# Kernel tuning notes

Hardware: AMD Instinct MI355X
Metric: run time of the kernel (lower is better)

## Reference

```python
import jax, jax.numpy as jnp
import numpy as np

N = 50000
E = 800000
NODE_F = 128
LIN = 128
HID = 32
HEADS = 2
OUT = 64
NCLS = 8
NEG_SLOPE = 0.2


def _lin_params(key, fan_in, fan_out, scale=0.05):
    k1, k2 = jax.random.split(key)
    W = jax.random.normal(k1, (fan_in, fan_out), jnp.float32) * scale
    b = jax.random.normal(k2, (fan_out,), jnp.float32) * scale
    return W, b


def setup_inputs() -> dict:
    key = jax.random.key(0)
    ks = jax.random.split(key, 12)
    h = jax.random.normal(ks[0], (N, NODE_F), jnp.float32)
    edge_w = jax.random.uniform(ks[1], (E,), jnp.float32, 1e-3, 1.0)
    src = jax.random.randint(ks[2], (E,), 0, N, jnp.int32)
    dst = jax.random.randint(ks[3], (E,), 0, N, jnp.int32)
    Wn, bn = _lin_params(ks[4], NODE_F, LIN)
    W1s, b1s = _lin_params(ks[5], LIN, HEADS * HID)
    W1d, b1d = _lin_params(ks[6], LIN, HEADS * HID)
    attn1 = jax.random.normal(ks[7], (HEADS, HID), jnp.float32) * 0.05
    W2s, b2s = _lin_params(ks[8], HEADS * HID, OUT)
    W2d, b2d = _lin_params(ks[9], HEADS * HID, OUT)
    attn2 = jax.random.normal(ks[10], (1, OUT), jnp.float32) * 0.05
    k11, k12, k13 = jax.random.split(ks[11], 3)
    Wc1, bc1 = _lin_params(k11, OUT, OUT // 2)
    Wc2, bc2 = _lin_params(k12, OUT // 2, OUT // 4)
    Wcls, bcls = _lin_params(k13, 2 * (OUT // 4), NCLS)
    return dict(h=h, edge_w=edge_w, src=src, dst=dst, Wn=Wn, bn=bn,
                W1s=W1s, b1s=b1s, W1d=W1d, b1d=b1d, attn1=attn1,
                W2s=W2s, b2s=b2s, W2d=W2d, b2d=b2d, attn2=attn2,
                Wc1=Wc1, bc1=bc1, Wc2=Wc2, bc2=bc2, Wcls=Wcls, bcls=bcls)


def _segment_softmax(logits, seg, num_segments):
    # logits: [E, H], seg: [E] destination node ids
    m = jax.ops.segment_max(logits, seg, num_segments=num_segments)
    e = jnp.exp(logits - m[seg])
    s = jax.ops.segment_sum(e, seg, num_segments=num_segments)
    return e / s[seg]


def _gatv2(x, src, dst, Ws, bs, Wd, bd, attn, heads, dim):
    n = x.shape[0]
    fs = (x @ Ws + bs).reshape(n, heads, dim)
    fd = (x @ Wd + bd).reshape(n, heads, dim)
    e = jax.nn.leaky_relu(fs[src] + fd[dst], NEG_SLOPE)  # [E,H,D]
    logits = jnp.einsum('ehd,hd->eh', e, attn)
    alpha = _segment_softmax(logits, dst, n)  # [E,H]
    return jax.ops.segment_sum(fs[src] * alpha[..., None], dst, num_segments=n)


def _forward(h, edge_w, src, dst, Wn, bn, W1s, b1s, W1d, b1d, attn1,
             W2s, b2s, W2d, b2d, attn2, Wc1, bc1, Wc2, bc2, Wcls, bcls):
    n = h.shape[0]
    # EdgeWeightNorm(norm='both'): w / sqrt(out_wdeg(src) * in_wdeg(dst))
    out_wdeg = jax.ops.segment_sum(edge_w, src, num_segments=n)
    in_wdeg = jax.ops.segment_sum(edge_w, dst, num_segments=n)
    norm_w = edge_w * jax.lax.rsqrt(out_wdeg[src]) * jax.lax.rsqrt(in_wdeg[dst])

    node_f = h @ Wn + bn
    # GATv2 layer 1 (dropout is identity in eval)
    g1 = _gatv2(node_f, src, dst, W1s, b1s, W1d, b1d, attn1, HEADS, HID)
    x = jax.nn.elu(g1).reshape(n, HEADS * HID)
    # GATv2 layer 2 (single head)
    g2 = _gatv2(x, src, dst, W2s, b2s, W2d, b2d, attn2, 1, OUT)
    x = jax.nn.elu(g2).reshape(n, OUT)

    # GraphConv norm='none' with edge_weight: sum_in(w * (xW)[src]) + b
    xm = x @ Wc1
    c1 = jax.ops.segment_sum(xm[src] * norm_w[:, None], dst, num_segments=n) + bc1
    x = jax.nn.elu(c1)

    # GraphConv norm='both' (unweighted degrees, clamped to >=1)
    ones_e = jnp.ones((src.shape[0],), x.dtype)
    dout = jnp.clip(jax.ops.segment_sum(ones_e, src, num_segments=n), 1.0)
    din = jnp.clip(jax.ops.segment_sum(ones_e, dst, num_segments=n), 1.0)
    xs = (x @ Wc2) * jax.lax.rsqrt(dout)[:, None]
    c2 = jax.ops.segment_sum(xs[src], dst, num_segments=n) * jax.lax.rsqrt(din)[:, None] + bc2
    x = jax.nn.elu(c2)

    # MLPPredictor: per-edge score from concat(src, dst) features
    score = jnp.concatenate([x[src], x[dst]], axis=1) @ Wcls + bcls
    return score


def reference(h, edge_w, src, dst, Wn, bn, W1s, b1s, W1d, b1d, attn1,
              W2s, b2s, W2d, b2d, attn2, Wc1, bc1, Wc2, bc2, Wcls, bcls):
    return _forward(h, edge_w, src, dst, Wn, bn, W1s, b1s, W1d, b1d, attn1,
                    W2s, b2s, W2d, b2d, attn2, Wc1, bc1, Wc2, bc2, Wcls, bcls)
```

## Files before the change

kernel.cpp:

```cpp
#include <hip/hip_runtime.h>
#include <math.h>

#define NN 50000
#define NE 800000

__device__ __forceinline__ float elu1(float x) { return x > 0.f ? x : expm1f(x); }
__device__ __forceinline__ float lrelu(float x) { return x >= 0.f ? x : 0.2f * x; }

__global__ __launch_bounds__(256) void fat0_kernel(
    const float* __restrict__ Wn, const float* __restrict__ bn,
    const float* __restrict__ W1s, const float* __restrict__ b1s,
    const float* __restrict__ W1d, const float* __restrict__ b1d,
    float* __restrict__ Wns, float* __restrict__ Wnd,
    float* __restrict__ bns, float* __restrict__ bnd,
    float* __restrict__ zbase) {
  if (blockIdx.x < 65) {
    int t = blockIdx.x * 256 + threadIdx.x;
    if (t < 8192) {
      int i = t >> 6, o = t & 63;
      float acc = 0.f;
      for (int k = 0; k < 128; ++k) acc += Wn[i * 128 + k] * W1s[k * 64 + o];
      Wns[t] = acc;
    } else if (t < 16384) {
      int u = t - 8192;
      int i = u >> 6, o = u & 63;
      float acc = 0.f;
      for (int k = 0; k < 128; ++k) acc += Wn[i * 128 + k] * W1d[k * 64 + o];
      Wnd[u] = acc;
    } else if (t < 16448) {
      int o = t - 16384;
      float acc = b1s[o];
      for (int k = 0; k < 128; ++k) acc += bn[k] * W1s[k * 64 + o];
      bns[o] = acc;
    } else if (t < 16512) {
      int o = t - 16448;
      float acc = b1d[o];
      for (int k = 0; k < 128; ++k) acc += bn[k] * W1d[k * 64 + o];
      bnd[o] = acc;
    }
  } else {
    int i = (blockIdx.x - 65) * 256 + threadIdx.x;
    if (i < 3 * NN) zbase[i] = 0.f;
  }
}

__global__ __launch_bounds__(256) void edge_rank(const int* __restrict__ dst,
                                                 int* __restrict__ cnt,
                                                 int* __restrict__ rank) {
  int e = blockIdx.x * blockDim.x + threadIdx.x;
  if (e >= NE) return;
  rank[e] = atomicAdd(&cnt[dst[e]], 1);
}

__global__ __launch_bounds__(1024) void scan_all(const int* __restrict__ cnt,
                                                 int* __restrict__ row_start) {
  __shared__ int sh[1024];
  int t = threadIdx.x;
  const int CHUNK = (NN + 1023) / 1024;
  int base = t * CHUNK;
  int lim = base + CHUNK;
  if (lim > NN) lim = NN;
  int s = 0;
#pragma unroll 8
  for (int i = base; i < lim; ++i) s += cnt[i];
  sh[t] = s;
  __syncthreads();
  for (int off = 1; off < 1024; off <<= 1) {
    int add = (t >= off) ? sh[t - off] : 0;
    __syncthreads();
    sh[t] += add;
    __syncthreads();
  }
  int run = sh[t] - s;
#pragma unroll 8
  for (int i = base; i < lim; ++i) {
    row_start[i] = run;
    run += cnt[i];
  }
  if (base < NN && base + CHUNK >= NN) row_start[NN] = run;
}

template <int K, int M, bool ELU_IN, int RS, bool DUAL>
__device__ __forceinline__ void gemm_body(int blk, float* __restrict__ xs,
                                          const float* __restrict__ X,
                                          const float* __restrict__ W1,
                                          const float* __restrict__ b1,
                                          const float* __restrict__ W2,
                                          const float* __restrict__ b2,
                                          const float* __restrict__ cnt,
                                          float* __restrict__ Y1,
                                          float* __restrict__ Y2) {
  constexpr int RPT = 4;
  constexpr int ROWS = (256 / M) * RPT;
  int row0 = blk * ROWS;
  int t = threadIdx.x;
  for (int idx = t; idx < ROWS * K; idx += 256) {
    int r = idx / K, k = idx - r * K;
    int row = row0 + r;
    float v = (row < NN) ? X[row * K + k] : 0.f;
    if (ELU_IN) v = elu1(v);
    xs[r * K + k] = v;
  }
  __syncthreads();
  int m = t % M, rg = t / M;
  int rbase = rg * RPT;
  float acc1[RPT], acc2[RPT];
#pragma unroll
  for (int j = 0; j < RPT; ++j) {
    acc1[j] = b1 ? b1[m] : 0.f;
    if (DUAL) acc2[j] = b2 ? b2[m] : 0.f;
  }
#pragma unroll 4
  for (int k = 0; k < K; ++k) {
    float w1 = W1[k * M + m];
    float w2 = DUAL ? W2[k * M + m] : 0.f;
#pragma unroll
    for (int j = 0; j < RPT; ++j) {
      float x = xs[(rbase + j) * K + k];
      acc1[j] += x * w1;
      if (DUAL) acc2[j] += x * w2;
    }
  }
#pragma unroll
  for (int j = 0; j < RPT; ++j) {
    int row = row0 + rbase + j;
    if (row >= NN) continue;
    float sc = 1.f;
    if (RS == 1) sc = rsqrtf(fmaxf(cnt[row], 1.f));
    if (RS == 2) {
      float wv = cnt[row];
      sc = (wv > 0.f) ? rsqrtf(wv) : 0.f;
    }
    Y1[row * M + m] = acc1[j] * sc;
    if (DUAL) Y2[row * M + m] = acc2[j] * sc;
  }
}

template <int K, int M, bool ELU_IN, int RS, bool DUAL>
__global__ __launch_bounds__(256) void node_gemm(const float* __restrict__ X,
                                                 const float* __restrict__ W1,
                                                 const float* __restrict__ b1,
                                                 const float* __restrict__ W2,
                                                 const float* __restrict__ b2,
                                                 const float* __restrict__ cnt,
                                                 float* __restrict__ Y1,
                                                 float* __restrict__ Y2) {
  __shared__ float xs[(256 / M) * 4 * K];
  gemm_body<K, M, ELU_IN, RS, DUAL>(blockIdx.x, xs, X, W1, b1, W2, b2, cnt, Y1, Y2);
}

__global__ __launch_bounds__(256) void fatB_kernel(
    const int* __restrict__ src, const int* __restrict__ dst,
    const float* __restrict__ ew, const int* __restrict__ row_start,
    const int* __restrict__ rank, int2* __restrict__ psrcw,
    unsigned long long* __restrict__ degw,
    const float* __restrict__ h, const float* __restrict__ Wns,
    const float* __restrict__ bns, const float* __restrict__ Wnd,
    const float* __restrict__ bnd, float* __restrict__ FS, float* __restrict__ FD) {
  __shared__ float xs[16 * 128];
  int c = blockIdx.x >> 1;
  if (blockIdx.x & 1) {
    gemm_body<128, 64, false, 0, true>(c, xs, h, Wns, bns, Wnd, bnd, nullptr, FS, FD);
  } else {
    int e = c * 256 + threadIdx.x;
    if (e >= NE) return;
    int s = src[e], d = dst[e];
    float w = ew[e];
    psrcw[row_start[d] + rank[e]] = make_int2(s, __float_as_int(w));
    unsigned long long pk = (1ULL << 44) | (unsigned long long)(w * 4294967296.0f);
    atomicAdd(&degw[s], pk);
  }
}

__global__ __launch_bounds__(256) void fatL2_kernel(
    const float* __restrict__ G, const float* __restrict__ W2s,
    const float* __restrict__ b2s, const float* __restrict__ W2d,
    const float* __restrict__ b2d, float* __restrict__ FS, float* __restrict__ FD,
    const unsigned long long* __restrict__ degw, float* __restrict__ deg) {
  __shared__ float xs[16 * 64];
  if (blockIdx.x < 3125) {
    gemm_body<64, 64, true, 0, true>(blockIdx.x, xs, G, W2s, b2s, W2d, b2d, nullptr, FS, FD);
  } else {
    int i = (blockIdx.x - 3125) * 256 + threadIdx.x;
    if (i >= NN) return;
    unsigned long long v = degw[i];
    deg[i] = (float)((double)(v & ((1ULL << 44) - 1)) * (1.0 / 4294967296.0));
    deg[NN + i] = (float)(v >> 44);
  }
}

template <int HALFW>
__global__ __launch_bounds__(256) void gat_fused(const int* __restrict__ row_start,
                                                 const int2* __restrict__ psrcw,
                                                 const float* __restrict__ fs,
                                                 const float* __restrict__ fd,
                                                 const float* __restrict__ attn,
                                                 float* __restrict__ g) {
  int n = blockIdx.x * 4 + (threadIdx.x >> 6);
  if (n >= NN) return;
  int lane = threadIdx.x & 63;
  int beg = row_start[n], end = row_start[n + 1];
  float fdv = fd[n * 64 + lane];
  float av = attn[lane];
  float acc = 0.f, den = 0.f;
  int i = beg;
  for (; i + 3 < end; i += 4) {
    int s0 = psrcw[i].x, s1 = psrcw[i + 1].x, s2 = psrcw[i + 2].x, s3 = psrcw[i + 3].x;
    float f0 = fs[s0 * 64 + lane];
    float f1 = fs[s1 * 64 + lane];
    float f2 = fs[s2 * 64 + lane];
    float f3 = fs[s3 * 64 + lane];
    float v0 = lrelu(f0 + fdv) * av;
    float v1 = lrelu(f1 + fdv) * av;
    float v2 = lrelu(f2 + fdv) * av;
    float v3 = lrelu(f3 + fdv) * av;
#pragma unroll
    for (int m = 16; m >= 1; m >>= 1) {
      v0 += __shfl_xor(v0, m, 64);
      v1 += __shfl_xor(v1, m, 64);
      v2 += __shfl_xor(v2, m, 64);
      v3 += __shfl_xor(v3, m, 64);
    }
    if (!HALFW) {
      v0 += __shfl_xor(v0, 32, 64);
      v1 += __shfl_xor(v1, 32, 64);
      v2 += __shfl_xor(v2, 32, 64);
      v3 += __shfl_xor(v3, 32, 64);
    }
    float p0 = __expf(v0);
    float p1 = __expf(v1);
    float p2 = __expf(v2);
    float p3 = __expf(v3);
    acc += f0 * p0 + f1 * p1 + f2 * p2 + f3 * p3;
    den += p0 + p1 + p2 + p3;
  }
  for (; i < end; ++i) {
    int s = psrcw[i].x;
    float fsv = fs[s * 64 + lane];
    float v = lrelu(fsv + fdv) * av;
#pragma unroll
    for (int m = 16; m >= 1; m >>= 1) v += __shfl_xor(v, m, 64);
    if (!HALFW) v += __shfl_xor(v, 32, 64);
    float p = __expf(v);
    acc += fsv * p;
    den += p;
  }
  g[n * 64 + lane] = (end > beg) ? acc / den : 0.f;
}

__global__ __launch_bounds__(256) void gconv1_fused(const int* __restrict__ row_start,
                                                    const int2* __restrict__ psrcw,
                                                    const float* __restrict__ ym,
                                                    const float* __restrict__ bc1,
                                                    float* __restrict__ x3a) {
  int n = blockIdx.x * 4 + (threadIdx.x >> 6);
  if (n >= NN) return;
  int lane = threadIdx.x & 63;
  int half = lane >> 5, f = lane & 31;
  int beg = row_start[n], end = row_start[n + 1];
  float acc = 0.f, wsum = 0.f;
  int i = beg + half;
  for (; i + 2 < end; i += 4) {
    int2 a = psrcw[i], b = psrcw[i + 2];
    float wa = __int_as_float(a.y), wb = __int_as_float(b.y);
    acc += ym[a.x * 32 + f] * wa + ym[b.x * 32 + f] * wb;
    wsum += wa + wb;
  }
  if (i < end) {
    int2 a = psrcw[i];
    float wa = __int_as_float(a.y);
    acc += ym[a.x * 32 + f] * wa;
    wsum += wa;
  }
  acc += __shfl_xor(acc, 32, 64);
  wsum += __shfl_xor(wsum, 32, 64);
  if (lane < 32) {
    float r = (end > beg) ? acc * rsqrtf(wsum) : 0.f;
    x3a[n * 32 + lane] = elu1(r + bc1[lane]);
  }
}

__global__ __launch_bounds__(256) void gconv2_fused(const int* __restrict__ row_start,
                                                    const int2* __restrict__ psrcw,
                                                    const float* __restrict__ xs,
                                                    const float* __restrict__ bc2,
                                                    float* __restrict__ x4) {
  int n = blockIdx.x * 4 + (threadIdx.x >> 6);
  if (n >= NN) return;
  int lane = threadIdx.x & 63;
  int q = lane >> 4, f = lane & 15;
  int beg = row_start[n], end = row_start[n + 1];
  float acc = 0.f;
  int i = beg + q;
  for (; i + 4 < end; i += 8) acc += xs[psrcw[i].x * 16 + f] + xs[psrcw[i + 4].x * 16 + f];
  if (i < end) acc += xs[psrcw[i].x * 16 + f];
  acc += __shfl_xor(acc, 16, 64);
  acc += __shfl_xor(acc, 32, 64);
  if (lane < 16) {
    float len = (float)(end - beg);
    x4[n * 16 + lane] = elu1(acc * rsqrtf(fmaxf(len, 1.f)) + bc2[lane]);
  }
}

__global__ __launch_bounds__(256) void classifier_kernel(const int* __restrict__ src,
                                                         const int* __restrict__ dst,
                                                         const float* __restrict__ x4,
                                                         const float* __restrict__ Wcls,
                                                         const float* __restrict__ bcls,
                                                         float* __restrict__ out) {
  __shared__ float w[256];
  __shared__ float bb[8];
  if (threadIdx.x < 256) w[threadIdx.x] = Wcls[threadIdx.x];
  if (threadIdx.x < 8) bb[threadIdx.x] = bcls[threadIdx.x];
  __syncthreads();
  int t = blockIdx.x * blockDim.x + threadIdx.x;
  int e = t >> 1, c0 = (t & 1) * 4;
  if (e >= NE) return;
  int s = src[e], d = dst[e];
  const float4* xsv = (const float4*)&x4[s * 16];
  const float4* xdv = (const float4*)&x4[d * 16];
  float acc0 = bb[c0], acc1 = bb[c0 + 1], acc2 = bb[c0 + 2], acc3 = bb[c0 + 3];
#pragma unroll
  for (int q = 0; q < 4; ++q) {
    float4 xv = xsv[q];
#pragma unroll
    for (int j = 0; j < 4; ++j) {
      float x = j == 0 ? xv.x : j == 1 ? xv.y : j == 2 ? xv.z : xv.w;
      const float* wr = &w[(q * 4 + j) * 8 + c0];
      acc0 += x * wr[0];
      acc1 += x * wr[1];
      acc2 += x * wr[2];
      acc3 += x * wr[3];
    }
  }
#pragma unroll
  for (int q = 0; q < 4; ++q) {
    float4 xv = xdv[q];
#pragma unroll
    for (int j = 0; j < 4; ++j) {
      float x = j == 0 ? xv.x : j == 1 ? xv.y : j == 2 ? xv.z : xv.w;
      const float* wr = &w[(16 + q * 4 + j) * 8 + c0];
      acc0 += x * wr[0];
      acc1 += x * wr[1];
      acc2 += x * wr[2];
      acc3 += x * wr[3];
    }
  }
  *(float4*)&out[e * 8 + c0] = make_float4(acc0, acc1, acc2, acc3);
}

extern "C" void kernel_launch(void* const* d_in, const int* in_sizes, int n_in,
                              void* d_out, int out_size, void* d_ws, size_t ws_size,
                              hipStream_t stream) {
  const float* h      = (const float*)d_in[0];
  const float* edge_w = (const float*)d_in[1];
  const int*   src    = (const int*)d_in[2];
  const int*   dst    = (const int*)d_in[3];
  const float* Wn    = (const float*)d_in[4];
  const float* bn    = (const float*)d_in[5];
  const float* W1s   = (const float*)d_in[6];
  const float* b1s   = (const float*)d_in[7];
  const float* W1d   = (const float*)d_in[8];
  const float* b1d   = (const float*)d_in[9];
  const float* attn1 = (const float*)d_in[10];
  const float* W2s   = (const float*)d_in[11];
  const float* b2s   = (const float*)d_in[12];
  const float* W2d   = (const float*)d_in[13];
  const float* b2d   = (const float*)d_in[14];
  const float* attn2 = (const float*)d_in[15];
  const float* Wc1   = (const float*)d_in[16];
  const float* bc1   = (const float*)d_in[17];
  const float* Wc2   = (const float*)d_in[18];
  const float* bc2   = (const float*)d_in[19];
  const float* Wcls  = (const float*)d_in[20];
  const float* bcls  = (const float*)d_in[21];
  float* out = (float*)d_out;

  float* ws = (float*)d_ws;
  size_t off = 0;
  auto alloc = [&](size_t nf) { float* pp = ws + off; off += (nf + 3) & ~(size_t)3; return pp; };
  float* Wns = alloc(8192);
  float* Wnd = alloc(8192);
  float* bns = alloc(64);
  float* bnd = alloc(64);
  unsigned long long* degw = (unsigned long long*)alloc(2 * NN);
  int*   cnt = (int*)alloc(NN);
  float* deg = alloc(2 * NN);
  int*   row_start = (int*)alloc(NN + 1);
  int2*  psrcw = (int2*)alloc(2 * NE);
  float* FS  = alloc(64 * NN);
  float* FD  = alloc(64 * NN);
  float* G   = alloc(64 * NN);
  int*   rank = (int*)G;

  dim3 b256(256);
  const int EB = (NE + 255) / 256;
  const int NB4 = (NN + 3) / 4;

  fat0_kernel<<<65 + (3 * NN + 255) / 256, b256, 0, stream>>>(
      Wn, bn, W1s, b1s, W1d, b1d, Wns, Wnd, bns, bnd, (float*)degw);
  edge_rank<<<EB, b256, 0, stream>>>(dst, cnt, rank);
  scan_all<<<1, 1024, 0, stream>>>(cnt, row_start);
  fatB_kernel<<<2 * EB, b256, 0, stream>>>(src, dst, edge_w, row_start, rank, psrcw,
                                           degw, h, Wns, bns, Wnd, bnd, FS, FD);
  gat_fused<1><<<NB4, b256, 0, stream>>>(row_start, psrcw, FS, FD, attn1, G);
  fatL2_kernel<<<3125 + (NN + 255) / 256, b256, 0, stream>>>(G, W2s, b2s, W2d, b2d,
                                                             FS, FD, degw, deg);
  gat_fused<0><<<NB4, b256, 0, stream>>>(row_start, psrcw, FS, FD, attn2, G);
  node_gemm<64, 32, true, 2, false><<<(NN + 31) / 32, b256, 0, stream>>>(
      G, Wc1, nullptr, nullptr, nullptr, deg, FS, nullptr);
  gconv1_fused<<<NB4, b256, 0, stream>>>(row_start, psrcw, FS, bc1, FD);
  node_gemm<32, 16, false, 1, false><<<(NN + 63) / 64, b256, 0, stream>>>(
      FD, Wc2, nullptr, nullptr, nullptr, deg + NN, FS, nullptr);
  gconv2_fused<<<NB4, b256, 0, stream>>>(row_start, psrcw, FS, bc2, G);
  classifier_kernel<<<(NE * 2 + 255) / 256, b256, 0, stream>>>(src, dst, G, Wcls, bcls, out);
}
```

Baseline: 491.1 us.

## Fuse Wc1/Wc2 node GEMMs into aggregation kernels and merge edge ranking

The two small node GEMMs for Wc1 and Wc2 are folded into the epilogues of the second GAT aggregation and the first graph-conv kernel. Each folds in with lane shuffles against weights staged in LDS, applying the degree rsqrt scaling there. This removes two launches and a round-trip of intermediate node features through global memory. Edge ranking is merged into the first setup kernel, which needs a separate small kernel to zero the counts first. The GAT edge loop is also unrolled from 4 to 8 edges per iteration to keep more gathers in flight, at the cost of more registers and extra per-node shuffle work in the epilogue.

```diff
diff --git a/kernel.cpp b/kernel.cpp
--- a/kernel.cpp
+++ b/kernel.cpp
@@ -7,14 +7,22 @@
 __device__ __forceinline__ float elu1(float x) { return x > 0.f ? x : expm1f(x); }
 __device__ __forceinline__ float lrelu(float x) { return x >= 0.f ? x : 0.2f * x; }
 
-__global__ __launch_bounds__(256) void fat0_kernel(
+__global__ __launch_bounds__(256) void zero_cnt(int* __restrict__ cnt) {
+  int i = blockIdx.x * blockDim.x + threadIdx.x;
+  if (i < NN) cnt[i] = 0;
+}
+
+#define FATA_CB 65
+#define FATA_ZB 391
+__global__ __launch_bounds__(256) void fatA_kernel(
     const float* __restrict__ Wn, const float* __restrict__ bn,
     const float* __restrict__ W1s, const float* __restrict__ b1s,
     const float* __restrict__ W1d, const float* __restrict__ b1d,
     float* __restrict__ Wns, float* __restrict__ Wnd,
     float* __restrict__ bns, float* __restrict__ bnd,
-    float* __restrict__ zbase) {
-  if (blockIdx.x < 65) {
+    float* __restrict__ degw_z,
+    const int* __restrict__ dst, int* __restrict__ cnt, int* __restrict__ rank) {
+  if (blockIdx.x < FATA_CB) {
     int t = blockIdx.x * 256 + threadIdx.x;
     if (t < 8192) {
       int i = t >> 6, o = t & 63;
@@ -38,18 +46,13 @@
       for (int k = 0; k < 128; ++k) acc += bn[k] * W1d[k * 64 + o];
       bnd[o] = acc;
     }
+  } else if (blockIdx.x < FATA_CB + FATA_ZB) {
+    int i = (blockIdx.x - FATA_CB) * 256 + threadIdx.x;
+    if (i < 2 * NN) degw_z[i] = 0.f;
   } else {
-    int i = (blockIdx.x - 65) * 256 + threadIdx.x;
-    if (i < 3 * NN) zbase[i] = 0.f;
-  }
-}
-
-__global__ __launch_bounds__(256) void edge_rank(const int* __restrict__ dst,
-                                                 int* __restrict__ cnt,
-                                                 int* __restrict__ rank) {
-  int e = blockIdx.x * blockDim.x + threadIdx.x;
-  if (e >= NE) return;
-  rank[e] = atomicAdd(&cnt[dst[e]], 1);
+    int e = (blockIdx.x - FATA_CB - FATA_ZB) * 256 + threadIdx.x;
+    if (e < NE) rank[e] = atomicAdd(&cnt[dst[e]], 1);
+  }
 }
 
 __global__ __launch_bounds__(1024) void scan_all(const int* __restrict__ cnt,
@@ -80,14 +83,13 @@
   if (base < NN && base + CHUNK >= NN) row_start[NN] = run;
 }
 
-template <int K, int M, bool ELU_IN, int RS, bool DUAL>
+template <int K, int M, bool ELU_IN, bool DUAL>
 __device__ __forceinline__ void gemm_body(int blk, float* __restrict__ xs,
                                           const float* __restrict__ X,
                                           const float* __restrict__ W1,
                                           const float* __restrict__ b1,
                                           const float* __restrict__ W2,
                                           const float* __restrict__ b2,
-                                          const float* __restrict__ cnt,
                                           float* __restrict__ Y1,
                                           float* __restrict__ Y2) {
   constexpr int RPT = 4;
@@ -125,28 +127,9 @@
   for (int j = 0; j < RPT; ++j) {
     int row = row0 + rbase + j;
     if (row >= NN) continue;
-    float sc = 1.f;
-    if (RS == 1) sc = rsqrtf(fmaxf(cnt[row], 1.f));
-    if (RS == 2) {
-      float wv = cnt[row];
-      sc = (wv > 0.f) ? rsqrtf(wv) : 0.f;
-    }
-    Y1[row * M + m] = acc1[j] * sc;
-    if (DUAL) Y2[row * M + m] = acc2[j] * sc;
-  }
-}
-
-template <int K, int M, bool ELU_IN, int RS, bool DUAL>
-__global__ __launch_bounds__(256) void node_gemm(const float* __restrict__ X,
-                                                 const float* __restrict__ W1,
-                                                 const float* __restrict__ b1,
-                                                 const float* __restrict__ W2,
-                                                 const float* __restrict__ b2,
-                                                 const float* __restrict__ cnt,
-                                                 float* __restrict__ Y1,
-                                                 float* __restrict__ Y2) {
-  __shared__ float xs[(256 / M) * 4 * K];
-  gemm_body<K, M, ELU_IN, RS, DUAL>(blockIdx.x, xs, X, W1, b1, W2, b2, cnt, Y1, Y2);
+    Y1[row * M + m] = acc1[j];
+    if (DUAL) Y2[row * M + m] = acc2[j];
+  }
 }
 
 __global__ __launch_bounds__(256) void fatB_kernel(
@@ -160,7 +143,7 @@
   __shared__ float xs[16 * 128];
   int c = blockIdx.x >> 1;
   if (blockIdx.x & 1) {
-    gemm_body<128, 64, false, 0, true>(c, xs, h, Wns, bns, Wnd, bnd, nullptr, FS, FD);
+    gemm_body<128, 64, false, true>(c, xs, h, Wns, bns, Wnd, bnd, FS, FD);
   } else {
     int e = c * 256 + threadIdx.x;
     if (e >= NE) return;
@@ -179,7 +162,7 @@
     const unsigned long long* __restrict__ degw, float* __restrict__ deg) {
   __shared__ float xs[16 * 64];
   if (blockIdx.x < 3125) {
-    gemm_body<64, 64, true, 0, true>(blockIdx.x, xs, G, W2s, b2s, W2d, b2d, nullptr, FS, FD);
+    gemm_body<64, 64, true, true>(blockIdx.x, xs, G, W2s, b2s, W2d, b2d, FS, FD);
   } else {
     int i = (blockIdx.x - 3125) * 256 + threadIdx.x;
     if (i >= NN) return;
@@ -189,50 +172,48 @@
   }
 }
 
-template <int HALFW>
+template <int HALFW, int FUSE_YM>
 __global__ __launch_bounds__(256) void gat_fused(const int* __restrict__ row_start,
                                                  const int2* __restrict__ psrcw,
                                                  const float* __restrict__ fs,
                                                  const float* __restrict__ fd,
                                                  const float* __restrict__ attn,
+                                                 const float* __restrict__ Wc1,
+                                                 const float* __restrict__ wdeg_out,
                                                  float* __restrict__ g) {
+  __shared__ float wlds[FUSE_YM ? 64 * 32 : 1];
+  if (FUSE_YM) {
+    for (int idx = threadIdx.x; idx < 2048; idx += 256) wlds[idx] = Wc1[idx];
+    __syncthreads();
+  }
   int n = blockIdx.x * 4 + (threadIdx.x >> 6);
-  if (n >= NN) return;
   int lane = threadIdx.x & 63;
   int beg = row_start[n], end = row_start[n + 1];
   float fdv = fd[n * 64 + lane];
   float av = attn[lane];
   float acc = 0.f, den = 0.f;
   int i = beg;
-  for (; i + 3 < end; i += 4) {
-    int s0 = psrcw[i].x, s1 = psrcw[i + 1].x, s2 = psrcw[i + 2].x, s3 = psrcw[i + 3].x;
-    float f0 = fs[s0 * 64 + lane];
-    float f1 = fs[s1 * 64 + lane];
-    float f2 = fs[s2 * 64 + lane];
-    float f3 = fs[s3 * 64 + lane];
-    float v0 = lrelu(f0 + fdv) * av;
-    float v1 = lrelu(f1 + fdv) * av;
-    float v2 = lrelu(f2 + fdv) * av;
-    float v3 = lrelu(f3 + fdv) * av;
+  for (; i + 7 < end; i += 8) {
+    float f[8], v[8];
+#pragma unroll
+    for (int j = 0; j < 8; ++j) f[j] = fs[psrcw[i + j].x * 64 + lane];
+#pragma unroll
+    for (int j = 0; j < 8; ++j) v[j] = lrelu(f[j] + fdv) * av;
 #pragma unroll
     for (int m = 16; m >= 1; m >>= 1) {
-      v0 += __shfl_xor(v0, m, 64);
-      v1 += __shfl_xor(v1, m, 64);
-      v2 += __shfl_xor(v2, m, 64);
-      v3 += __shfl_xor(v3, m, 64);
+#pragma unroll
+      for (int j = 0; j < 8; ++j) v[j] += __shfl_xor(v[j], m, 64);
     }
     if (!HALFW) {
-      v0 += __shfl_xor(v0, 32, 64);
-      v1 += __shfl_xor(v1, 32, 64);
-      v2 += __shfl_xor(v2, 32, 64);
-      v3 += __shfl_xor(v3, 32, 64);
-    }
-    float p0 = __expf(v0);
-    float p1 = __expf(v1);
-    float p2 = __expf(v2);
-    float p3 = __expf(v3);
-    acc += f0 * p0 + f1 * p1 + f2 * p2 + f3 * p3;
-    den += p0 + p1 + p2 + p3;
+#pragma unroll
+      for (int j = 0; j < 8; ++j) v[j] += __shfl_xor(v[j], 32, 64);
+    }
+#pragma unroll
+    for (int j = 0; j < 8; ++j) {
+      float p = __expf(v[j]);
+      acc += f[j] * p;
+      den += p;
+    }
   }
   for (; i < end; ++i) {
     int s = psrcw[i].x;
@@ -245,16 +226,33 @@
     acc += fsv * p;
     den += p;
   }
-  g[n * 64 + lane] = (end > beg) ? acc / den : 0.f;
-}
-
-__global__ __launch_bounds__(256) void gconv1_fused(const int* __restrict__ row_start,
-                                                    const int2* __restrict__ psrcw,
-                                                    const float* __restrict__ ym,
-                                                    const float* __restrict__ bc1,
-                                                    float* __restrict__ x3a) {
+  float gv = (end > beg) ? acc / den : 0.f;
+  if (!FUSE_YM) {
+    g[n * 64 + lane] = gv;
+  } else {
+    float xv = elu1(gv);
+    float accm = 0.f;
+#pragma unroll 8
+    for (int k = 0; k < 64; ++k) accm += __shfl(xv, k, 64) * wlds[k * 32 + (lane & 31)];
+    if (lane < 32) {
+      float wv = wdeg_out[n];
+      float rs = (wv > 0.f) ? rsqrtf(wv) : 0.f;
+      g[n * 32 + lane] = accm * rs;
+    }
+  }
+}
+
+__global__ __launch_bounds__(256) void gconv1x_kernel(const int* __restrict__ row_start,
+                                                      const int2* __restrict__ psrcw,
+                                                      const float* __restrict__ ym,
+                                                      const float* __restrict__ bc1,
+                                                      const float* __restrict__ Wc2,
+                                                      const float* __restrict__ cnt_out,
+                                                      float* __restrict__ xsout) {
+  __shared__ float w2[32 * 16];
+  for (int idx = threadIdx.x; idx < 512; idx += 256) w2[idx] = Wc2[idx];
+  __syncthreads();
   int n = blockIdx.x * 4 + (threadIdx.x >> 6);
-  if (n >= NN) return;
   int lane = threadIdx.x & 63;
   int half = lane >> 5, f = lane & 31;
   int beg = row_start[n], end = row_start[n + 1];
@@ -274,10 +272,11 @@
   }
   acc += __shfl_xor(acc, 32, 64);
   wsum += __shfl_xor(wsum, 32, 64);
-  if (lane < 32) {
-    float r = (end > beg) ? acc * rsqrtf(wsum) : 0.f;
-    x3a[n * 32 + lane] = elu1(r + bc1[lane]);
-  }
+  float x3v = elu1(((end > beg) ? acc * rsqrtf(wsum) : 0.f) + bc1[f]);
+  float accm = 0.f;
+#pragma unroll 8
+  for (int k = 0; k < 32; ++k) accm += __shfl(x3v, k, 64) * w2[k * 16 + (lane & 15)];
+  if (lane < 16) xsout[n * 16 + lane] = accm * rsqrtf(fmaxf(cnt_out[n], 1.f));
 }
 
 __global__ __launch_bounds__(256) void gconv2_fused(const int* __restrict__ row_start,
@@ -397,21 +396,19 @@
   const int EB = (NE + 255) / 256;
   const int NB4 = (NN + 3) / 4;
 
-  fat0_kernel<<<65 + (3 * NN + 255) / 256, b256, 0, stream>>>(
-      Wn, bn, W1s, b1s, W1d, b1d, Wns, Wnd, bns, bnd, (float*)degw);
-  edge_rank<<<EB, b256, 0, stream>>>(dst, cnt, rank);
+  zero_cnt<<<(NN + 255) / 256, b256, 0, stream>>>(cnt);
+  fatA_kernel<<<FATA_CB + FATA_ZB + EB, b256, 0, stream>>>(
+      Wn, bn, W1s, b1s, W1d, b1d, Wns, Wnd, bns, bnd, (float*)degw, dst, cnt, rank);
   scan_all<<<1, 1024, 0, stream>>>(cnt, row_start);
   fatB_kernel<<<2 * EB, b256, 0, stream>>>(src, dst, edge_w, row_start, rank, psrcw,
                                            degw, h, Wns, bns, Wnd, bnd, FS, FD);
-  gat_fused<1><<<NB4, b256, 0, stream>>>(row_start, psrcw, FS, FD, attn1, G);
+  gat_fused<1, 0><<<NB4, b256, 0, stream>>>(row_start, psrcw, FS, FD, attn1,
+                                            nullptr, nullptr, G);
   fatL2_kernel<<<3125 + (NN + 255) / 256, b256, 0, stream>>>(G, W2s, b2s, W2d, b2d,
                                                              FS, FD, degw, deg);
-  gat_fused<0><<<NB4, b256, 0, stream>>>(row_start, psrcw, FS, FD, attn2, G);
-  node_gemm<64, 32, true, 2, false><<<(NN + 31) / 32, b256, 0, stream>>>(
-      G, Wc1, nullptr, nullptr, nullptr, deg, FS, nullptr);
-  gconv1_fused<<<NB4, b256, 0, stream>>>(row_start, psrcw, FS, bc1, FD);
-  node_gemm<32, 16, false, 1, false><<<(NN + 63) / 64, b256, 0, stream>>>(
-      FD, Wc2, nullptr, nullptr, nullptr, deg + NN, FS, nullptr);
-  gconv2_fused<<<NB4, b256, 0, stream>>>(row_start, psrcw, FS, bc2, G);
-  classifier_kernel<<<(NE * 2 + 255) / 256, b256, 0, stream>>>(src, dst, G, Wcls, bcls, out);
-}
+  gat_fused<0, 1><<<NB4, b256, 0, stream>>>(row_start, psrcw, FS, FD, attn2,
+                                            Wc1, deg, G);
+  gconv1x_kernel<<<NB4, b256, 0, stream>>>(row_start, psrcw, G, bc1, Wc2, deg + NN, FD);
+  gconv2_fused<<<NB4, b256, 0, stream>>>(row_start, psrcw, FD, bc2, FS);
+  classifier_kernel<<<(NE * 2 + 255) / 256, b256, 0, stream>>>(src, dst, FS, Wcls, bcls, out);
+}
```

Result: slower. 515.5 us (+5.0%).
